# Kernel tuning notes

Hardware: AMD Instinct MI355X
Metric: run time of the kernel (lower is better)

The kernel has to match this reference:

```python
import jax, jax.numpy as jnp
import numpy as np

B, G, O, N, T = 32, 16, 256, 88, 256


def setup_inputs() -> dict:
    key = jax.random.key(0)
    k1, k2, k3, k4, k5 = jax.random.split(key, 5)
    x = jax.random.normal(k1, (B, N, T), dtype=jnp.float32)
    y = jax.random.uniform(k2, (B, G), dtype=jnp.float32)  # soft genre weights
    weight = jax.random.normal(k3, (G, O, N, T), dtype=jnp.float32) * 0.05
    mask = (jax.random.uniform(k4, (O, T)) < 0.5).astype(jnp.float32)
    bias = jax.random.normal(k5, (O,), dtype=jnp.float32)
    return {"x": x, "y": y, "weight": weight, "mask": mask, "bias": bias}


def reference(x, y, weight, mask, bias):
    # Original: maskedWeight = einsum('gont,ot->gont'); genreWeight = einsum('bg,gont->bont');
    # out = einsum('bnt,bont->bno') + bias. Fused into one contraction (same math,
    # avoids materializing the [b,o,n,t] intermediate).
    out = jnp.einsum('bnt,bg,gont,ot->bno', x, y, weight, mask)
    return out + bias
```

## Files before the change

### kernel.cpp

```cpp
#include <hip/hip_runtime.h>

#define Bq 32
#define Gq 16
#define Oq 256
#define Nq 88
#define Tq 256

typedef short bf16x8 __attribute__((ext_vector_type(8)));
typedef float f32x4 __attribute__((ext_vector_type(4)));

static __device__ __forceinline__ short f2bf(float f) {
    return __builtin_bit_cast(short, (__bf16)f);
}

static __device__ __forceinline__ void gld_lds16(const float* src, float* lds_dst) {
    __builtin_amdgcn_global_load_lds(
        (const __attribute__((address_space(1))) void*)src,
        (__attribute__((address_space(3))) void*)lds_dst, 16, 0, 0);
}

__global__ __launch_bounds__(256, 4)
void mlm_mfma2(const float* __restrict__ x, const float* __restrict__ y,
               const float* __restrict__ w, const float* __restrict__ mask,
               const float* __restrict__ bias, float* __restrict__ out) {
    __shared__ float wbuf[2][4096];
    __shared__ float y_lds[512];

    const int n  = blockIdx.x >> 4;
    const int o0 = (blockIdx.x & 15) << 4;
    const int tid  = threadIdx.x;
    const int wv   = tid >> 6;
    const int lane = tid & 63;
    const int lo = lane & 15;
    const int hi = lane >> 4;
    const int sr = lo & 7;

    y_lds[tid]       = y[tid];
    y_lds[tid + 256] = y[tid + 256];

    bf16x8 afrag[2][2];
    f32x4 mka[2], mkb[2];
    const int tbase = wv * 64;
#pragma unroll
    for (int W = 0; W < 2; ++W) {
        const int ta = tbase + W * 32 + hi * 4;
        const int tb = ta + 16;
        f32x4 xa0 = *(const f32x4*)(x + ((size_t)lo * Nq + n) * Tq + ta);
        f32x4 xb0 = *(const f32x4*)(x + ((size_t)lo * Nq + n) * Tq + tb);
        f32x4 xa1 = *(const f32x4*)(x + ((size_t)(lo + 16) * Nq + n) * Tq + ta);
        f32x4 xb1 = *(const f32x4*)(x + ((size_t)(lo + 16) * Nq + n) * Tq + tb);
        mka[W] = *(const f32x4*)(mask + (size_t)(o0 + lo) * Tq + ta);
        mkb[W] = *(const f32x4*)(mask + (size_t)(o0 + lo) * Tq + tb);
#pragma unroll
        for (int j = 0; j < 4; ++j) {
            afrag[W][0][j]     = f2bf(xa0[j]);
            afrag[W][0][j + 4] = f2bf(xb0[j]);
            afrag[W][1][j]     = f2bf(xa1[j]);
            afrag[W][1][j + 4] = f2bf(xb1[j]);
        }
    }

    const size_t GS = (size_t)Oq * Nq * Tq;
    const float* wrow[4];
#pragma unroll
    for (int q = 0; q < 4; ++q) {
        const int r = wv * 4 + q;
        wrow[q] = w + ((size_t)(o0 + r) * Nq + n) * Tq;
    }

#pragma unroll
    for (int q = 0; q < 4; ++q) {
        const int r = wv * 4 + q;
        gld_lds16(wrow[q] + ((lane ^ (r & 7)) << 2), &wbuf[0][r * 256]);
    }
    asm volatile("s_waitcnt vmcnt(0)" ::: "memory");
    __syncthreads();

    f32x4 facc0 = {0.f, 0.f, 0.f, 0.f};
    f32x4 facc1 = {0.f, 0.f, 0.f, 0.f};

    for (int g = 0; g < 16; ++g) {
        const int cb = g & 1;
        if (g < 15) {
#pragma unroll
            for (int q = 0; q < 4; ++q) {
                const int r = wv * 4 + q;
                gld_lds16(wrow[q] + (size_t)(g + 1) * GS + ((lane ^ (r & 7)) << 2),
                          &wbuf[cb ^ 1][r * 256]);
            }
        }

        f32x4 acc0 = {0.f, 0.f, 0.f, 0.f};
        f32x4 acc1 = {0.f, 0.f, 0.f, 0.f};
#pragma unroll
        for (int W = 0; W < 2; ++W) {
            const int c0 = wv * 16 + W * 8 + hi;
            f32x4 wa4 = *(const f32x4*)&wbuf[cb][lo * 256 + ((c0 ^ sr) << 2)];
            f32x4 wb4 = *(const f32x4*)&wbuf[cb][lo * 256 + (((c0 + 4) ^ sr) << 2)];
            bf16x8 bfr;
#pragma unroll
            for (int j = 0; j < 4; ++j) {
                bfr[j]     = f2bf(wa4[j] * mka[W][j]);
                bfr[j + 4] = f2bf(wb4[j] * mkb[W][j]);
            }
            acc0 = __builtin_amdgcn_mfma_f32_16x16x32_bf16(afrag[W][0], bfr, acc0, 0, 0, 0);
            acc1 = __builtin_amdgcn_mfma_f32_16x16x32_bf16(afrag[W][1], bfr, acc1, 0, 0, 0);
        }

#pragma unroll
        for (int i = 0; i < 4; ++i) {
            facc0[i] += y_lds[(hi * 4 + i) * Gq + g] * acc0[i];
            facc1[i] += y_lds[(16 + hi * 4 + i) * Gq + g] * acc1[i];
        }

        asm volatile("s_waitcnt vmcnt(0)" ::: "memory");
        __syncthreads();
    }

    float (*red)[32][16] = (float (*)[32][16]) & wbuf[0][0];
#pragma unroll
    for (int i = 0; i < 4; ++i) {
        red[wv][hi * 4 + i][lo]      = facc0[i];
        red[wv][16 + hi * 4 + i][lo] = facc1[i];
    }
    __syncthreads();

#pragma unroll
    for (int s = 0; s < 2; ++s) {
        const int idx = tid + s * 256;
        const int b  = idx >> 4;
        const int oo = idx & 15;
        const float v = red[0][b][oo] + red[1][b][oo] + red[2][b][oo] + red[3][b][oo]
                      + bias[o0 + oo];
        out[((size_t)b * Nq + n) * Oq + o0 + oo] = v;
    }
}

extern "C" void kernel_launch(void* const* d_in, const int* in_sizes, int n_in,
                              void* d_out, int out_size, void* d_ws, size_t ws_size,
                              hipStream_t stream) {
    const float* x    = (const float*)d_in[0];
    const float* y    = (const float*)d_in[1];
    const float* w    = (const float*)d_in[2];
    const float* mask = (const float*)d_in[3];
    const float* bias = (const float*)d_in[4];
    float* out = (float*)d_out;

    dim3 grid(Nq * (Oq / 16));
    dim3 block(256);
    hipLaunchKernelGGL(mlm_mfma2, grid, block, 0, stream, x, y, w, mask, bias, out);
}
```

Baseline: 75.20 us.

## Process two n values per 512-thread block to reuse mask across n

```diff
diff --git a/kernel.cpp b/kernel.cpp
--- a/kernel.cpp
+++ b/kernel.cpp
@@ -19,15 +19,16 @@
         (__attribute__((address_space(3))) void*)lds_dst, 16, 0, 0);
 }
 
-__global__ __launch_bounds__(256, 4)
-void mlm_mfma2(const float* __restrict__ x, const float* __restrict__ y,
+__global__ __launch_bounds__(512, 4)
+void mlm_mfma3(const float* __restrict__ x, const float* __restrict__ y,
                const float* __restrict__ w, const float* __restrict__ mask,
                const float* __restrict__ bias, float* __restrict__ out) {
-    __shared__ float wbuf[2][4096];
+    __shared__ float wbuf[2][8192];
     __shared__ float y_lds[512];
 
-    const int n  = blockIdx.x >> 4;
-    const int o0 = (blockIdx.x & 15) << 4;
+    const int unit = blockIdx.x;
+    const int n0 = (unit >> 4) * 2;
+    const int o0 = (unit & 15) << 4;
     const int tid  = threadIdx.x;
     const int wv   = tid >> 6;
     const int lane = tid & 63;
@@ -35,104 +36,106 @@
     const int hi = lane >> 4;
     const int sr = lo & 7;
 
-    y_lds[tid]       = y[tid];
-    y_lds[tid + 256] = y[tid + 256];
+    y_lds[tid] = y[tid];
 
+    const int tA = wv * 32 + hi * 4;
+    const int tB = tA + 16;
+    f32x4 mka = *(const f32x4*)(mask + (size_t)(o0 + lo) * Tq + tA);
+    f32x4 mkb = *(const f32x4*)(mask + (size_t)(o0 + lo) * Tq + tB);
     bf16x8 afrag[2][2];
-    f32x4 mka[2], mkb[2];
-    const int tbase = wv * 64;
 #pragma unroll
-    for (int W = 0; W < 2; ++W) {
-        const int ta = tbase + W * 32 + hi * 4;
-        const int tb = ta + 16;
-        f32x4 xa0 = *(const f32x4*)(x + ((size_t)lo * Nq + n) * Tq + ta);
-        f32x4 xb0 = *(const f32x4*)(x + ((size_t)lo * Nq + n) * Tq + tb);
-        f32x4 xa1 = *(const f32x4*)(x + ((size_t)(lo + 16) * Nq + n) * Tq + ta);
-        f32x4 xb1 = *(const f32x4*)(x + ((size_t)(lo + 16) * Nq + n) * Tq + tb);
-        mka[W] = *(const f32x4*)(mask + (size_t)(o0 + lo) * Tq + ta);
-        mkb[W] = *(const f32x4*)(mask + (size_t)(o0 + lo) * Tq + tb);
+    for (int nn = 0; nn < 2; ++nn) {
+        f32x4 xa0 = *(const f32x4*)(x + ((size_t)lo * Nq + n0 + nn) * Tq + tA);
+        f32x4 xb0 = *(const f32x4*)(x + ((size_t)lo * Nq + n0 + nn) * Tq + tB);
+        f32x4 xa1 = *(const f32x4*)(x + ((size_t)(lo + 16) * Nq + n0 + nn) * Tq + tA);
+        f32x4 xb1 = *(const f32x4*)(x + ((size_t)(lo + 16) * Nq + n0 + nn) * Tq + tB);
 #pragma unroll
         for (int j = 0; j < 4; ++j) {
-            afrag[W][0][j]     = f2bf(xa0[j]);
-            afrag[W][0][j + 4] = f2bf(xb0[j]);
-            afrag[W][1][j]     = f2bf(xa1[j]);
-            afrag[W][1][j + 4] = f2bf(xb1[j]);
+            afrag[nn][0][j]     = f2bf(xa0[j]);
+            afrag[nn][0][j + 4] = f2bf(xb0[j]);
+            afrag[nn][1][j]     = f2bf(xa1[j]);
+            afrag[nn][1][j + 4] = f2bf(xb1[j]);
         }
     }
 
     const size_t GS = (size_t)Oq * Nq * Tq;
-    const float* wrow[4];
+    const float* wsrc[4];
 #pragma unroll
     for (int q = 0; q < 4; ++q) {
-        const int r = wv * 4 + q;
-        wrow[q] = w + ((size_t)(o0 + r) * Nq + n) * Tq;
+        const int i = wv * 4 + q, r = i >> 1, nn = i & 1;
+        wsrc[q] = w + ((size_t)(o0 + r) * Nq + n0 + nn) * Tq + ((lane ^ (r & 7)) << 2);
     }
 
 #pragma unroll
-    for (int q = 0; q < 4; ++q) {
-        const int r = wv * 4 + q;
-        gld_lds16(wrow[q] + ((lane ^ (r & 7)) << 2), &wbuf[0][r * 256]);
-    }
+    for (int q = 0; q < 4; ++q)
+        gld_lds16(wsrc[q], &wbuf[0][(wv * 4 + q) * 256]);
     asm volatile("s_waitcnt vmcnt(0)" ::: "memory");
     __syncthreads();
 
-    f32x4 facc0 = {0.f, 0.f, 0.f, 0.f};
-    f32x4 facc1 = {0.f, 0.f, 0.f, 0.f};
+    f32x4 facc[2][2] = {};
 
     for (int g = 0; g < 16; ++g) {
         const int cb = g & 1;
         if (g < 15) {
 #pragma unroll
-            for (int q = 0; q < 4; ++q) {
-                const int r = wv * 4 + q;
-                gld_lds16(wrow[q] + (size_t)(g + 1) * GS + ((lane ^ (r & 7)) << 2),
-                          &wbuf[cb ^ 1][r * 256]);
-            }
+            for (int q = 0; q < 4; ++q)
+                gld_lds16(wsrc[q] + (size_t)(g + 1) * GS,
+                          &wbuf[cb ^ 1][(wv * 4 + q) * 256]);
         }
 
-        f32x4 acc0 = {0.f, 0.f, 0.f, 0.f};
-        f32x4 acc1 = {0.f, 0.f, 0.f, 0.f};
+        float yv0[4], yv1[4];
 #pragma unroll
-        for (int W = 0; W < 2; ++W) {
-            const int c0 = wv * 16 + W * 8 + hi;
-            f32x4 wa4 = *(const f32x4*)&wbuf[cb][lo * 256 + ((c0 ^ sr) << 2)];
-            f32x4 wb4 = *(const f32x4*)&wbuf[cb][lo * 256 + (((c0 + 4) ^ sr) << 2)];
+        for (int i = 0; i < 4; ++i) {
+            yv0[i] = y_lds[(hi * 4 + i) * Gq + g];
+            yv1[i] = y_lds[(16 + hi * 4 + i) * Gq + g];
+        }
+
+        const int c0 = wv * 8 + hi;
+#pragma unroll
+        for (int nn = 0; nn < 2; ++nn) {
+            f32x4 wa4 = *(const f32x4*)&wbuf[cb][(lo * 2 + nn) * 256 + ((c0 ^ sr) << 2)];
+            f32x4 wb4 = *(const f32x4*)&wbuf[cb][(lo * 2 + nn) * 256 + (((c0 + 4) ^ sr) << 2)];
             bf16x8 bfr;
 #pragma unroll
             for (int j = 0; j < 4; ++j) {
-                bfr[j]     = f2bf(wa4[j] * mka[W][j]);
-                bfr[j + 4] = f2bf(wb4[j] * mkb[W][j]);
+                bfr[j]     = f2bf(wa4[j] * mka[j]);
+                bfr[j + 4] = f2bf(wb4[j] * mkb[j]);
             }
-            acc0 = __builtin_amdgcn_mfma_f32_16x16x32_bf16(afrag[W][0], bfr, acc0, 0, 0, 0);
-            acc1 = __builtin_amdgcn_mfma_f32_16x16x32_bf16(afrag[W][1], bfr, acc1, 0, 0, 0);
-        }
-
+            f32x4 z = {0.f, 0.f, 0.f, 0.f};
+            f32x4 a0 = __builtin_amdgcn_mfma_f32_16x16x32_bf16(afrag[nn][0], bfr, z, 0, 0, 0);
+            f32x4 a1 = __builtin_amdgcn_mfma_f32_16x16x32_bf16(afrag[nn][1], bfr, z, 0, 0, 0);
 #pragma unroll
-        for (int i = 0; i < 4; ++i) {
-            facc0[i] += y_lds[(hi * 4 + i) * Gq + g] * acc0[i];
-            facc1[i] += y_lds[(16 + hi * 4 + i) * Gq + g] * acc1[i];
+            for (int i = 0; i < 4; ++i) {
+                facc[nn][0][i] += yv0[i] * a0[i];
+                facc[nn][1][i] += yv1[i] * a1[i];
+            }
         }
 
         asm volatile("s_waitcnt vmcnt(0)" ::: "memory");
         __syncthreads();
     }
 
-    float (*red)[32][16] = (float (*)[32][16]) & wbuf[0][0];
+    float (*red)[2][32][16] = (float (*)[2][32][16]) & wbuf[0][0];
 #pragma unroll
     for (int i = 0; i < 4; ++i) {
-        red[wv][hi * 4 + i][lo]      = facc0[i];
-        red[wv][16 + hi * 4 + i][lo] = facc1[i];
+#pragma unroll
+        for (int nn = 0; nn < 2; ++nn) {
+            red[wv][nn][hi * 4 + i][lo]      = facc[nn][0][i];
+            red[wv][nn][16 + hi * 4 + i][lo] = facc[nn][1][i];
+        }
     }
     __syncthreads();
 
 #pragma unroll
     for (int s = 0; s < 2; ++s) {
-        const int idx = tid + s * 256;
-        const int b  = idx >> 4;
-        const int oo = idx & 15;
-        const float v = red[0][b][oo] + red[1][b][oo] + red[2][b][oo] + red[3][b][oo]
-                      + bias[o0 + oo];
-        out[((size_t)b * Nq + n) * Oq + o0 + oo] = v;
+        const int idx = tid + s * 512;
+        const int nn  = idx >> 9;
+        const int b   = (idx >> 4) & 31;
+        const int oo  = idx & 15;
+        float v = bias[o0 + oo];
+#pragma unroll
+        for (int p = 0; p < 8; ++p) v += red[p][nn][b][oo];
+        out[((size_t)b * Nq + n0 + nn) * Oq + o0 + oo] = v;
     }
 }
 
@@ -146,7 +149,7 @@
     const float* bias = (const float*)d_in[4];
     float* out = (float*)d_out;
 
-    dim3 grid(Nq * (Oq / 16));
-    dim3 block(256);
-    hipLaunchKernelGGL(mlm_mfma2, grid, block, 0, stream, x, y, w, mask, bias, out);
+    dim3 grid((Nq / 2) * (Oq / 16));
+    dim3 block(512);
+    hipLaunchKernelGGL(mlm_mfma3, grid, block, 0, stream, x, y, w, mask, bias, out);
 }
```

New measurement: 77.00 us. 1.02x slower.

## Split genre dimension across blocks with atomic accumulation and bf16 x pre-conversion

Applied to the files above, without the earlier changes.

```diff
diff --git a/kernel.cpp b/kernel.cpp
--- a/kernel.cpp
+++ b/kernel.cpp
@@ -7,6 +7,7 @@
 #define Tq 256
 
 typedef short bf16x8 __attribute__((ext_vector_type(8)));
+typedef short bf16x4 __attribute__((ext_vector_type(4)));
 typedef float f32x4 __attribute__((ext_vector_type(4)));
 
 static __device__ __forceinline__ short f2bf(float f) {
@@ -19,120 +20,137 @@
         (__attribute__((address_space(3))) void*)lds_dst, 16, 0, 0);
 }
 
-__global__ __launch_bounds__(256, 4)
-void mlm_mfma2(const float* __restrict__ x, const float* __restrict__ y,
+__global__ __launch_bounds__(256)
+void mlm_init(const float* __restrict__ bias, float* __restrict__ out) {
+    const int idx = blockIdx.x * 256 + threadIdx.x;
+    out[idx] = bias[idx & (Oq - 1)];
+}
+
+__global__ __launch_bounds__(256)
+void mlm_xcvt(const float* __restrict__ x, short* __restrict__ xbf) {
+    const int idx = blockIdx.x * 256 + threadIdx.x;
+    xbf[idx] = f2bf(x[idx]);
+}
+
+template <bool XBF>
+__global__ __launch_bounds__(256, 2)
+void mlm_split(const float* __restrict__ x, const short* __restrict__ xbf,
+               const float* __restrict__ y,
                const float* __restrict__ w, const float* __restrict__ mask,
-               const float* __restrict__ bias, float* __restrict__ out) {
-    __shared__ float wbuf[2][4096];
-    __shared__ float y_lds[512];
+               float* __restrict__ out) {
+    __shared__ float wslab[16][4][256];
 
-    const int n  = blockIdx.x >> 4;
-    const int o0 = (blockIdx.x & 15) << 4;
-    const int tid  = threadIdx.x;
-    const int wv   = tid >> 6;
+    const int bid = blockIdx.x;
+    const int nq = bid % 22;
+    const int gg = (bid / 22) & 15;
+    const int ot = bid / (22 * 16);
+    const int o0 = ot << 4;
+    const int n0 = nq << 2;
+
+    const int tid = threadIdx.x;
+    const int wv = tid >> 6;
     const int lane = tid & 63;
     const int lo = lane & 15;
     const int hi = lane >> 4;
     const int sr = lo & 7;
 
-    y_lds[tid]       = y[tid];
-    y_lds[tid + 256] = y[tid + 256];
+#pragma unroll
+    for (int q = 0; q < 4; ++q) {
+        const int r = wv * 4 + q;
+        const float* rowp = w + (((size_t)(gg * Oq + o0 + r)) * Nq + n0) * Tq
+                              + ((lane ^ (r & 7)) << 2);
+#pragma unroll
+        for (int nn = 0; nn < 4; ++nn)
+            gld_lds16(rowp + nn * Tq, &wslab[r][nn][0]);
+    }
 
-    bf16x8 afrag[2][2];
+    bf16x8 afr[4][2][2];
     f32x4 mka[2], mkb[2];
-    const int tbase = wv * 64;
 #pragma unroll
     for (int W = 0; W < 2; ++W) {
-        const int ta = tbase + W * 32 + hi * 4;
-        const int tb = ta + 16;
-        f32x4 xa0 = *(const f32x4*)(x + ((size_t)lo * Nq + n) * Tq + ta);
-        f32x4 xb0 = *(const f32x4*)(x + ((size_t)lo * Nq + n) * Tq + tb);
-        f32x4 xa1 = *(const f32x4*)(x + ((size_t)(lo + 16) * Nq + n) * Tq + ta);
-        f32x4 xb1 = *(const f32x4*)(x + ((size_t)(lo + 16) * Nq + n) * Tq + tb);
-        mka[W] = *(const f32x4*)(mask + (size_t)(o0 + lo) * Tq + ta);
-        mkb[W] = *(const f32x4*)(mask + (size_t)(o0 + lo) * Tq + tb);
+        const int tA = wv * 64 + W * 32 + hi * 4;
+        const int tB = tA + 16;
+        mka[W] = *(const f32x4*)(mask + (size_t)(o0 + lo) * Tq + tA);
+        mkb[W] = *(const f32x4*)(mask + (size_t)(o0 + lo) * Tq + tB);
 #pragma unroll
-        for (int j = 0; j < 4; ++j) {
-            afrag[W][0][j]     = f2bf(xa0[j]);
-            afrag[W][0][j + 4] = f2bf(xb0[j]);
-            afrag[W][1][j]     = f2bf(xa1[j]);
-            afrag[W][1][j + 4] = f2bf(xb1[j]);
+        for (int nn = 0; nn < 4; ++nn) {
+#pragma unroll
+            for (int half = 0; half < 2; ++half) {
+                const size_t xoff = ((size_t)(half * 16 + lo) * Nq + n0 + nn) * Tq;
+                if (XBF) {
+                    bf16x4 pa = *(const bf16x4*)(xbf + xoff + tA);
+                    bf16x4 pb = *(const bf16x4*)(xbf + xoff + tB);
+#pragma unroll
+                    for (int j = 0; j < 4; ++j) {
+                        afr[nn][half][W][j]     = pa[j];
+                        afr[nn][half][W][j + 4] = pb[j];
+                    }
+                } else {
+                    f32x4 xa = *(const f32x4*)(x + xoff + tA);
+                    f32x4 xb = *(const f32x4*)(x + xoff + tB);
+#pragma unroll
+                    for (int j = 0; j < 4; ++j) {
+                        afr[nn][half][W][j]     = f2bf(xa[j]);
+                        afr[nn][half][W][j + 4] = f2bf(xb[j]);
+                    }
+                }
+            }
         }
     }
 
-    const size_t GS = (size_t)Oq * Nq * Tq;
-    const float* wrow[4];
+    float yv0[4], yv1[4];
 #pragma unroll
-    for (int q = 0; q < 4; ++q) {
-        const int r = wv * 4 + q;
-        wrow[q] = w + ((size_t)(o0 + r) * Nq + n) * Tq;
+    for (int i = 0; i < 4; ++i) {
+        yv0[i] = y[(hi * 4 + i) * Gq + gg];
+        yv1[i] = y[(16 + hi * 4 + i) * Gq + gg];
     }
 
-#pragma unroll
-    for (int q = 0; q < 4; ++q) {
-        const int r = wv * 4 + q;
-        gld_lds16(wrow[q] + ((lane ^ (r & 7)) << 2), &wbuf[0][r * 256]);
-    }
     asm volatile("s_waitcnt vmcnt(0)" ::: "memory");
     __syncthreads();
 
-    f32x4 facc0 = {0.f, 0.f, 0.f, 0.f};
-    f32x4 facc1 = {0.f, 0.f, 0.f, 0.f};
-
-    for (int g = 0; g < 16; ++g) {
-        const int cb = g & 1;
-        if (g < 15) {
+    f32x4 acc[4][2] = {};
 #pragma unroll
-            for (int q = 0; q < 4; ++q) {
-                const int r = wv * 4 + q;
-                gld_lds16(wrow[q] + (size_t)(g + 1) * GS + ((lane ^ (r & 7)) << 2),
-                          &wbuf[cb ^ 1][r * 256]);
-            }
-        }
-
-        f32x4 acc0 = {0.f, 0.f, 0.f, 0.f};
-        f32x4 acc1 = {0.f, 0.f, 0.f, 0.f};
+    for (int nn = 0; nn < 4; ++nn) {
 #pragma unroll
         for (int W = 0; W < 2; ++W) {
             const int c0 = wv * 16 + W * 8 + hi;
-            f32x4 wa4 = *(const f32x4*)&wbuf[cb][lo * 256 + ((c0 ^ sr) << 2)];
-            f32x4 wb4 = *(const f32x4*)&wbuf[cb][lo * 256 + (((c0 + 4) ^ sr) << 2)];
+            f32x4 wa4 = *(const f32x4*)&wslab[lo][nn][(c0 ^ sr) << 2];
+            f32x4 wb4 = *(const f32x4*)&wslab[lo][nn][((c0 + 4) ^ sr) << 2];
             bf16x8 bfr;
 #pragma unroll
             for (int j = 0; j < 4; ++j) {
                 bfr[j]     = f2bf(wa4[j] * mka[W][j]);
                 bfr[j + 4] = f2bf(wb4[j] * mkb[W][j]);
             }
-            acc0 = __builtin_amdgcn_mfma_f32_16x16x32_bf16(afrag[W][0], bfr, acc0, 0, 0, 0);
-            acc1 = __builtin_amdgcn_mfma_f32_16x16x32_bf16(afrag[W][1], bfr, acc1, 0, 0, 0);
+            acc[nn][0] = __builtin_amdgcn_mfma_f32_16x16x32_bf16(afr[nn][0][W], bfr, acc[nn][0], 0, 0, 0);
+            acc[nn][1] = __builtin_amdgcn_mfma_f32_16x16x32_bf16(afr[nn][1][W], bfr, acc[nn][1], 0, 0, 0);
         }
+    }
 
+    __syncthreads();
+
+    float* red = &wslab[0][0][0];
+#pragma unroll
+    for (int nn = 0; nn < 4; ++nn) {
 #pragma unroll
         for (int i = 0; i < 4; ++i) {
-            facc0[i] += y_lds[(hi * 4 + i) * Gq + g] * acc0[i];
-            facc1[i] += y_lds[(16 + hi * 4 + i) * Gq + g] * acc1[i];
+            red[((wv * 4 + nn) * 32 + hi * 4 + i) * 16 + lo]      = yv0[i] * acc[nn][0][i];
+            red[((wv * 4 + nn) * 32 + 16 + hi * 4 + i) * 16 + lo] = yv1[i] * acc[nn][1][i];
         }
-
-        asm volatile("s_waitcnt vmcnt(0)" ::: "memory");
-        __syncthreads();
-    }
-
-    float (*red)[32][16] = (float (*)[32][16]) & wbuf[0][0];
-#pragma unroll
-    for (int i = 0; i < 4; ++i) {
-        red[wv][hi * 4 + i][lo]      = facc0[i];
-        red[wv][16 + hi * 4 + i][lo] = facc1[i];
     }
     __syncthreads();
 
 #pragma unroll
-    for (int s = 0; s < 2; ++s) {
-        const int idx = tid + s * 256;
-        const int b  = idx >> 4;
-        const int oo = idx & 15;
-        const float v = red[0][b][oo] + red[1][b][oo] + red[2][b][oo] + red[3][b][oo]
-                      + bias[o0 + oo];
-        out[((size_t)b * Nq + n) * Oq + o0 + oo] = v;
+    for (int s = 0; s < 8; ++s) {
+        const int e = s * 256 + tid;
+        const int nn = e >> 9;
+        const int b  = (e >> 4) & 31;
+        const int oo = e & 15;
+        float v = 0.f;
+#pragma unroll
+        for (int p = 0; p < 4; ++p)
+            v += red[((p * 4 + nn) * 32 + b) * 16 + oo];
+        unsafeAtomicAdd(&out[((size_t)b * Nq + n0 + nn) * Oq + o0 + oo], v);
     }
 }
 
@@ -146,7 +164,18 @@
     const float* bias = (const float*)d_in[4];
     float* out = (float*)d_out;
 
-    dim3 grid(Nq * (Oq / 16));
-    dim3 block(256);
-    hipLaunchKernelGGL(mlm_mfma2, grid, block, 0, stream, x, y, w, mask, bias, out);
+    const int xelems = Bq * Nq * Tq;
+    const bool use_bf = ws_size >= (size_t)xelems * 2;
+
+    hipLaunchKernelGGL(mlm_init, dim3(xelems / 256), dim3(256), 0, stream, bias, out);
+
+    if (use_bf) {
+        short* xbf = (short*)d_ws;
+        hipLaunchKernelGGL(mlm_xcvt, dim3(xelems / 256), dim3(256), 0, stream, x, xbf);
+        hipLaunchKernelGGL((mlm_split<true>), dim3(16 * 16 * 22), dim3(256), 0, stream,
+                           x, xbf, y, w, mask, out);
+    } else {
+        hipLaunchKernelGGL((mlm_split<false>), dim3(16 * 16 * 22), dim3(256), 0, stream,
+                           x, (const short*)nullptr, y, w, mask, out);
+    }
 }
```

Result: slower. 142.8 us (+89.9%).

## Triple-buffer weight loads with prefetch distance two and swizzle block order

Applied to the files above, without the earlier changes.

```diff
diff --git a/kernel.cpp b/kernel.cpp
--- a/kernel.cpp
+++ b/kernel.cpp
@@ -19,15 +19,18 @@
         (__attribute__((address_space(3))) void*)lds_dst, 16, 0, 0);
 }
 
-__global__ __launch_bounds__(256, 4)
-void mlm_mfma2(const float* __restrict__ x, const float* __restrict__ y,
+__global__ __launch_bounds__(256, 3)
+void mlm_mfma5(const float* __restrict__ x, const float* __restrict__ y,
                const float* __restrict__ w, const float* __restrict__ mask,
                const float* __restrict__ bias, float* __restrict__ out) {
-    __shared__ float wbuf[2][4096];
+    __shared__ float wbuf[3][4096];
     __shared__ float y_lds[512];
 
-    const int n  = blockIdx.x >> 4;
-    const int o0 = (blockIdx.x & 15) << 4;
+    const int bid = blockIdx.x;
+    const int swz = (bid & 7) * ((Nq * 16) / 8) + (bid >> 3);
+    const int n  = swz >> 4;
+    const int o0 = (swz & 15) << 4;
+
     const int tid  = threadIdx.x;
     const int wv   = tid >> 6;
     const int lane = tid & 63;
@@ -61,33 +64,36 @@
     }
 
     const size_t GS = (size_t)Oq * Nq * Tq;
-    const float* wrow[4];
+    const float* wsrc[4];
 #pragma unroll
     for (int q = 0; q < 4; ++q) {
         const int r = wv * 4 + q;
-        wrow[q] = w + ((size_t)(o0 + r) * Nq + n) * Tq;
+        wsrc[q] = w + ((size_t)(o0 + r) * Nq + n) * Tq + ((lane ^ (r & 7)) << 2);
     }
 
+    __syncthreads();
+
 #pragma unroll
-    for (int q = 0; q < 4; ++q) {
-        const int r = wv * 4 + q;
-        gld_lds16(wrow[q] + ((lane ^ (r & 7)) << 2), &wbuf[0][r * 256]);
-    }
-    asm volatile("s_waitcnt vmcnt(0)" ::: "memory");
-    __syncthreads();
+    for (int q = 0; q < 4; ++q)
+        gld_lds16(wsrc[q], &wbuf[0][(wv * 4 + q) * 256]);
+#pragma unroll
+    for (int q = 0; q < 4; ++q)
+        gld_lds16(wsrc[q] + GS, &wbuf[1][(wv * 4 + q) * 256]);
+    asm volatile("s_waitcnt vmcnt(4)" ::: "memory");
+    __builtin_amdgcn_s_barrier();
 
     f32x4 facc0 = {0.f, 0.f, 0.f, 0.f};
     f32x4 facc1 = {0.f, 0.f, 0.f, 0.f};
 
+#pragma unroll
     for (int g = 0; g < 16; ++g) {
-        const int cb = g & 1;
-        if (g < 15) {
+        const int cb = g % 3;
+        if (g < 14) {
+            const int pb = (g + 2) % 3;
 #pragma unroll
-            for (int q = 0; q < 4; ++q) {
-                const int r = wv * 4 + q;
-                gld_lds16(wrow[q] + (size_t)(g + 1) * GS + ((lane ^ (r & 7)) << 2),
-                          &wbuf[cb ^ 1][r * 256]);
-            }
+            for (int q = 0; q < 4; ++q)
+                gld_lds16(wsrc[q] + (size_t)(g + 2) * GS,
+                          &wbuf[pb][(wv * 4 + q) * 256]);
         }
 
         f32x4 acc0 = {0.f, 0.f, 0.f, 0.f};
@@ -113,10 +119,16 @@
             facc1[i] += y_lds[(16 + hi * 4 + i) * Gq + g] * acc1[i];
         }
 
-        asm volatile("s_waitcnt vmcnt(0)" ::: "memory");
-        __syncthreads();
+        if (g < 14) {
+            asm volatile("s_waitcnt vmcnt(4)" ::: "memory");
+            __builtin_amdgcn_s_barrier();
+        } else if (g == 14) {
+            asm volatile("s_waitcnt vmcnt(0)" ::: "memory");
+            __builtin_amdgcn_s_barrier();
+        }
     }
 
+    __syncthreads();
     float (*red)[32][16] = (float (*)[32][16]) & wbuf[0][0];
 #pragma unroll
     for (int i = 0; i < 4; ++i) {
@@ -148,5 +160,5 @@
 
     dim3 grid(Nq * (Oq / 16));
     dim3 block(256);
-    hipLaunchKernelGGL(mlm_mfma2, grid, block, 0, stream, x, y, w, mask, bias, out);
+    hipLaunchKernelGGL(mlm_mfma5, grid, block, 0, stream, x, y, w, mask, bias, out);
 }
```

Measured after the change: 136.5 us. 1.82x slower.
